# Kernel optimization log

Hardware: AMD Instinct MI355X
Metric: run time of the kernel (lower is better)

Reference implementation:

```python
import jax, jax.numpy as jnp
import numpy as np

MAX_NUM_CAPS = 10
NEG = -1e9

def _layernorm(x, g, b):
    m = x.mean(-1, keepdims=True)
    v = x.var(-1, keepdims=True)
    return (x - m) / jnp.sqrt(v + 1e-5) * g + b

def _gatv2(x, Wl, Wr, att, bias, adj):
    # x: [B,M,F]; Wl/Wr: [F,H*C]; att: [H,C]; adj: [B,M,M] bool, adj[b,i,j] = edge i->j
    B, M, F = x.shape
    H, C = att.shape
    xl = jnp.einsum('bmf,fhc->bmhc', x, Wl.reshape(F, H, C))  # source transform
    xr = jnp.einsum('bmf,fhc->bmhc', x, Wr.reshape(F, H, C))  # target transform
    # GATv2 score: att . leaky_relu(xl[i] + xr[j]) for edge (src=i, dst=j)
    z = jax.nn.leaky_relu(xl[:, :, None, :, :] + xr[:, None, :, :, :], 0.2)  # [B,i,j,H,C]
    e = jnp.einsum('bijhc,hc->bijh', z, att)
    e = jnp.where(adj[..., None], e, NEG)
    alpha = jax.nn.softmax(e, axis=1)  # softmax over incoming sources i per target j
    out = jnp.einsum('bijh,bihc->bjhc', alpha, xl)  # aggregate at targets
    return out.reshape(B, M, H * C) + bias

def setup_inputs() -> dict:
    key = jax.random.key(0)
    ks = jax.random.split(key, 16)
    B, N, T = 128, 16, 48
    Fm, H, C3 = 128, 4, 64
    s = 0.05
    inp = {
        'team_obs': jax.random.normal(ks[0], (B, N, 14), jnp.float32),
        'target_obs': jax.random.normal(ks[1], (B, T, 15), jnp.float32),
        'team_mask': jax.random.normal(ks[2], (B, 2, N), jnp.float32),
        'local_target_mask': jnp.ones((B, T + 1), jnp.float32),
        'W_emb': jax.random.normal(ks[3], (16, Fm), jnp.float32) * s,
        'b_emb': jnp.zeros((Fm,), jnp.float32),
        'Wl1': jax.random.normal(ks[4], (Fm, Fm), jnp.float32) * s,
        'Wr1': jax.random.normal(ks[5], (Fm, Fm), jnp.float32) * s,
        'att1': jax.random.normal(ks[6], (H, Fm // H), jnp.float32) * s,
        'b1': jnp.zeros((Fm,), jnp.float32),
        'Wl2': jax.random.normal(ks[7], (Fm, Fm), jnp.float32) * s,
        'Wr2': jax.random.normal(ks[8], (Fm, Fm), jnp.float32) * s,
        'att2': jax.random.normal(ks[9], (H, Fm // H), jnp.float32) * s,
        'b2': jnp.zeros((Fm,), jnp.float32),
        'Wl3': jax.random.normal(ks[10], (Fm, C3), jnp.float32) * s,
        'Wr3': jax.random.normal(ks[11], (Fm, C3), jnp.float32) * s,
        'att3': jax.random.normal(ks[12], (1, C3), jnp.float32) * s,
        'b3': jnp.zeros((C3,), jnp.float32),
        'ln1_g': jnp.ones((Fm,), jnp.float32),
        'ln1_b': jnp.zeros((Fm,), jnp.float32),
        'ln2_g': jnp.ones((Fm,), jnp.float32),
        'ln2_b': jnp.zeros((Fm,), jnp.float32),
    }
    return inp

def reference(team_obs, target_obs, team_mask, local_target_mask,
              W_emb, b_emb, Wl1, Wr1, att1, b1, Wl2, Wr2, att2, b2,
              Wl3, Wr3, att3, b3, ln1_g, ln1_b, ln2_g, ln2_b):
    B, N, _ = team_obs.shape
    team = jnp.concatenate([team_obs, jnp.zeros((B, N, 2), team_obs.dtype)], axis=2)
    tgt = target_obs[:, :, :-1]
    T = tgt.shape[1]
    tgt = jnp.concatenate([tgt[:, :, :2 + MAX_NUM_CAPS],
                           jnp.zeros((B, T, 2), tgt.dtype),
                           tgt[:, :, -2:]], axis=2)
    fin = jnp.concatenate([team, tgt], axis=1)  # [B, M, inp_dim]
    h = fin @ W_emb + b_emb  # [B, M, 128]
    imp_team = team_mask[:, 0] != -1e9          # [B, N]
    imp_tgt = local_target_mask[:, :-1] != 0.0  # [B, T]
    imp = jnp.concatenate([imp_team, imp_tgt], axis=1)  # [B, M]
    M = N + T
    eye = jnp.eye(M, dtype=bool)
    # edges among active nodes minus diagonal; PyG GATv2Conv add_self_loops=True re-adds self edges
    adj = (imp[:, :, None] & imp[:, None, :] & ~eye) | eye  # [B, M, M]
    out = jax.nn.relu(_layernorm(_gatv2(h, Wl1, Wr1, att1, b1, adj), ln1_g, ln1_b))
    out = jax.nn.relu(_layernorm(_gatv2(out, Wl2, Wr2, att2, b2, adj), ln2_g, ln2_b))
    out = _gatv2(out, Wl3, Wr3, att3, b3, adj)
    return out  # [B, M, out_dim]
```

## Files before the change

kernel.cpp:

```cpp
#include <hip/hip_runtime.h>

typedef unsigned short u16;
typedef unsigned int   u32;
typedef _Float16 h2  __attribute__((ext_vector_type(2)));
typedef __fp16   hw2 __attribute__((ext_vector_type(2)));
typedef __fp16   hw8 __attribute__((ext_vector_type(8)));
typedef float    f4  __attribute__((ext_vector_type(4)));

#define XS 136
#define PS 72
#define BS 72
#define OS 72

static __device__ __forceinline__ h2 pk(float a, float b) {
    return __builtin_bit_cast(h2, __builtin_amdgcn_cvt_pkrtz(a, b));
}
static __device__ __forceinline__ float dot2(h2 a, h2 b, float c) {
    return __builtin_amdgcn_fdot2(__builtin_bit_cast(hw2, a),
                                  __builtin_bit_cast(hw2, b), c, false);
}
static __device__ __forceinline__ h2  b2h(u32 v) { return __builtin_bit_cast(h2, v); }
static __device__ __forceinline__ u32 h2u(h2 v)  { return __builtin_bit_cast(u32, v); }
static __device__ __forceinline__ h2  abs2(h2 v) { return b2h(h2u(v) & 0x7fff7fffu); }
static __device__ __forceinline__ u16 f2h(float f) { return __builtin_bit_cast(u16, (_Float16)f); }
static __device__ __forceinline__ f4 mfma16(uint4 a, uint4 b, f4 c) {
    return __builtin_amdgcn_mfma_f32_16x16x32_f16(__builtin_bit_cast(hw8, a),
                                                  __builtin_bit_cast(hw8, b), c, 0, 0, 0);
}

__global__ void pack_weights(const float* __restrict__ Wl1, const float* __restrict__ Wr1,
                             const float* __restrict__ Wl2, const float* __restrict__ Wr2,
                             const float* __restrict__ Wl3, const float* __restrict__ Wr3,
                             u32* __restrict__ wpk)
{
    const int o = blockIdx.x * 256 + threadIdx.x;
    const float* src; u32* dst; int local; int N;
    if      (o < 8192)  { src = Wl1; dst = wpk;         local = o;         N = 128; }
    else if (o < 16384) { src = Wr1; dst = wpk + 8192;  local = o - 8192;  N = 128; }
    else if (o < 24576) { src = Wl2; dst = wpk + 16384; local = o - 16384; N = 128; }
    else if (o < 32768) { src = Wr2; dst = wpk + 24576; local = o - 24576; N = 128; }
    else if (o < 36864) { src = Wl3; dst = wpk + 32768; local = o - 32768; N = 64;  }
    else                { src = Wr3; dst = wpk + 36864; local = o - 36864; N = 64;  }
    const int i2   = local & 3;
    const int lane = (local >> 2) & 63;
    const int frag = local >> 8;
    const int kb   = frag & 3;
    const int nt   = frag >> 2;
    const int k0   = kb*32 + ((lane >> 4) << 3) + i2*2;
    const int n    = nt*16 + (lane & 15);
    dst[local] = h2u(pk(src[k0*N + n], src[(k0+1)*N + n]));
}

static __device__ __forceinline__ void compute_imp(int t, int b,
    const float* __restrict__ team_mask, const float* __restrict__ ltm, float* sImp)
{
    if (t < 64) {
        float im;
        if (t < 16) im = (team_mask[b*32 + t] != -1000000000.0f) ? 1.f : 0.f;
        else        im = (ltm[b*49 + (t-16)] != 0.0f) ? 1.f : 0.f;
        sImp[t] = im;
    }
}

static __device__ __forceinline__ void matmul128(int w, int lane,
    const u32* __restrict__ wpkL, const u32* __restrict__ wpkR,
    const u16* sX, u16* sXl, uint4* sXrP, u16* sXlB)
{
    const int  mt  = w & 3;
    const bool isR = (w >= 4);
    const u32* wp  = isR ? wpkR : wpkL;
    const int  n15 = lane & 15;
    const int  qd  = lane >> 4;
    uint4 afr[4];
#pragma unroll
    for (int kb = 0; kb < 4; kb++)
        afr[kb] = *(const uint4*)&sX[(mt*16 + n15)*XS + kb*32 + (qd << 3)];
#pragma unroll
    for (int nt = 0; nt < 8; nt++) {
        f4 acc = {0.f, 0.f, 0.f, 0.f};
#pragma unroll
        for (int kb = 0; kb < 4; kb++) {
            uint4 bf = *(const uint4*)&wp[((nt*4 + kb)*64 + lane)*4];
            acc = mfma16(afr[kb], bf, acc);
        }
        const int n  = nt*16 + n15;
        const int mb = mt*16 + (qd << 2);
        if (!isR) {
#pragma unroll
            for (int r = 0; r < 4; r++) sXl[(mb + r)*XS + n] = f2h(acc[r]);
            uint2 u;
            u.x = h2u(pk(acc[0], acc[1]));
            u.y = h2u(pk(acc[2], acc[3]));
            *(uint2*)&sXlB[n*BS + mb] = u;
        } else {
            u16* xp = (u16*)sXrP;
#pragma unroll
            for (int r = 0; r < 4; r++)
                xp[(((n >> 3)*64) + mb + r)*8 + (n & 7)] = f2h(acc[r]);
        }
    }
}

static __device__ __forceinline__ void attn_scores(int w, int lane,
    const float* __restrict__ att,
    const u16* sXl, const uint4* sXrP, u16* sP,
    float* sAl, float* sL2, const float* sImp)
{
    const int h  = w & 3;
    const int hf = w >> 2;
    const int j  = lane;

    h2 a2[16];
#pragma unroll
    for (int q = 0; q < 16; q++) a2[q] = pk(att[h*32 + 2*q], att[h*32 + 2*q + 1]);

    if (w < 4) {
        const uint4* pr = (const uint4*)&sXl[lane*XS + h*32];
        float al = 0.f;
#pragma unroll
        for (int c4 = 0; c4 < 4; c4++) {
            uint4 v = pr[c4];
            al = dot2(b2h(v.x), a2[c4*4+0], al);
            al = dot2(b2h(v.y), a2[c4*4+1], al);
            al = dot2(b2h(v.z), a2[c4*4+2], al);
            al = dot2(b2h(v.w), a2[c4*4+3], al);
        }
        sAl[h*64 + lane] = al;
    }

    h2 xr2[16];
#pragma unroll
    for (int s = 0; s < 4; s++) {
        uint4 v = sXrP[(h*4 + s)*64 + j];
        xr2[s*4+0] = b2h(v.x); xr2[s*4+1] = b2h(v.y);
        xr2[s*4+2] = b2h(v.z); xr2[s*4+3] = b2h(v.w);
    }
    float Ar = 0.f;
#pragma unroll
    for (int q = 0; q < 16; q++) Ar = dot2(a2[q], xr2[q], Ar);
    const float impj = sImp[j];
    __syncthreads();

    float l = 0.f;
    uint4* pd = (uint4*)&sP[(h*64 + j)*PS + hf*32];
    for (int c8 = 0; c8 < 4; c8++) {
        u32 pr4[4];
        float pprev = 0.f;
#pragma unroll
        for (int i2 = 0; i2 < 8; i2++) {
            const int i = hf*32 + c8*8 + i2;
            const uint4* pl = (const uint4*)&sXl[i*XS + h*32];
            uint4 v0 = pl[0], v1 = pl[1], v2 = pl[2], v3 = pl[3];
            h2 xl2[16];
            xl2[0] = b2h(v0.x); xl2[1] = b2h(v0.y); xl2[2]  = b2h(v0.z); xl2[3]  = b2h(v0.w);
            xl2[4] = b2h(v1.x); xl2[5] = b2h(v1.y); xl2[6]  = b2h(v1.z); xl2[7]  = b2h(v1.w);
            xl2[8] = b2h(v2.x); xl2[9] = b2h(v2.y); xl2[10] = b2h(v2.z); xl2[11] = b2h(v2.w);
            xl2[12]= b2h(v3.x); xl2[13]= b2h(v3.y); xl2[14] = b2h(v3.z); xl2[15] = b2h(v3.w);
            float S0 = 0.f, S1 = 0.f;
#pragma unroll
            for (int q = 0; q < 16; q += 2) {
                h2 t0 = abs2(xl2[q]   + xr2[q]);
                h2 t1 = abs2(xl2[q+1] + xr2[q+1]);
                S0 = dot2(a2[q],   t0, S0);
                S1 = dot2(a2[q+1], t1, S1);
            }
            float e  = 0.6f*(sAl[h*64 + i] + Ar) + 0.4f*(S0 + S1);
            float ad = (i == j) ? 1.f : impj * sImp[i];
            float p  = (ad != 0.f) ? __expf(e) : 0.f;
            if (i2 & 1) {
                h2 pp = pk(pprev, p);
                pr4[i2 >> 1] = h2u(pp);
                l += (float)pp[0] + (float)pp[1];
            } else {
                pprev = p;
            }
        }
        pd[c8] = make_uint4(pr4[0], pr4[1], pr4[2], pr4[3]);
    }
    sL2[h*128 + hf*64 + j] = l;
}

static __device__ __forceinline__ void attn_agg_ln(int w, int lane,
    const float* __restrict__ bias, const float* __restrict__ lg, const float* __restrict__ lb,
    const u16* sP, const u16* sXlB, float* sOutF, const float* sL2,
    float* sPart, u16* sXout)
{
    const int h   = w & 3;
    const int jh2 = w >> 2;
    const int n15 = lane & 15;
    const int kq  = lane >> 4;

    f4 acc00 = {0.f,0.f,0.f,0.f}, acc01 = acc00, acc10 = acc00, acc11 = acc00;
#pragma unroll
    for (int ks = 0; ks < 2; ks++) {
        uint4 af0 = *(const uint4*)&sP[(h*64 + (jh2*2+0)*16 + n15)*PS + ks*32 + kq*8];
        uint4 af1 = *(const uint4*)&sP[(h*64 + (jh2*2+1)*16 + n15)*PS + ks*32 + kq*8];
        uint4 bf0 = *(const uint4*)&sXlB[(h*32 +  0 + n15)*BS + ks*32 + kq*8];
        uint4 bf1 = *(const uint4*)&sXlB[(h*32 + 16 + n15)*BS + ks*32 + kq*8];
        acc00 = mfma16(af0, bf0, acc00);
        acc01 = mfma16(af0, bf1, acc01);
        acc10 = mfma16(af1, bf0, acc10);
        acc11 = mfma16(af1, bf1, acc11);
    }
    {
        const int jb0 = jh2*32 + kq*4;
#pragma unroll
        for (int r = 0; r < 4; r++) {
            sOutF[(h*32 +  0 + n15)*OS + jb0 + r]      = acc00[r];
            sOutF[(h*32 + 16 + n15)*OS + jb0 + r]      = acc01[r];
            sOutF[(h*32 +  0 + n15)*OS + jb0 + 16 + r] = acc10[r];
            sOutF[(h*32 + 16 + n15)*OS + jb0 + 16 + r] = acc11[r];
        }
    }
    __syncthreads();

    const int cg = w, j = lane, hh = w >> 1;
    const float l  = sL2[hh*128 + j] + sL2[hh*128 + 64 + j];
    const float rl = 1.f / l;
    float y[16];
    float s1 = 0.f, s2 = 0.f;
#pragma unroll
    for (int k = 0; k < 16; k++) {
        float v = fmaf(sOutF[(cg*16 + k)*OS + j], rl, bias[cg*16 + k]);
        y[k] = v; s1 += v; s2 = fmaf(v, v, s2);
    }
    sPart[cg*64 + j] = s1;
    sPart[512 + cg*64 + j] = s2;
    __syncthreads();
    float su = 0.f, sq = 0.f;
#pragma unroll
    for (int p = 0; p < 8; p++) { su += sPart[p*64 + j]; sq += sPart[512 + p*64 + j]; }
    const float mean = su * 0.0078125f;
    const float var  = sq * 0.0078125f - mean*mean;
    const float rstd = rsqrtf(var + 1e-5f);
    u32* xo = (u32*)&sXout[j*XS];
#pragma unroll
    for (int q = 0; q < 8; q++) {
        const int c0 = cg*16 + 2*q;
        float v0 = fmaxf(fmaf((y[2*q]   - mean)*rstd, lg[c0],   lb[c0]),   0.f);
        float v1 = fmaxf(fmaf((y[2*q+1] - mean)*rstd, lg[c0+1], lb[c0+1]), 0.f);
        xo[cg*8 + q] = h2u(pk(v0, v1));
    }
}

__global__ void __launch_bounds__(512, 1) gnn_fused(
    const float* __restrict__ team_obs, const float* __restrict__ target_obs,
    const float* __restrict__ team_mask, const float* __restrict__ ltm,
    const float* __restrict__ W_emb, const float* __restrict__ b_emb,
    const float* __restrict__ att1, const float* __restrict__ b1,
    const float* __restrict__ ln1_g, const float* __restrict__ ln1_b,
    const float* __restrict__ att2, const float* __restrict__ b2,
    const float* __restrict__ ln2_g, const float* __restrict__ ln2_b,
    const float* __restrict__ att3, const float* __restrict__ b3,
    const u32* __restrict__ wpk, float* __restrict__ out)
{
    __shared__ __align__(16) u16   sX  [64*XS];
    __shared__ __align__(16) u16   sXl [64*XS];
    __shared__ __align__(16) uint4 sXrP[1024];
    __shared__ __align__(16) u16   sXlB[128*BS];
    __shared__ __align__(16) u16   sP  [4*64*PS];
    __shared__ __align__(16) float sOutF[128*OS];
    __shared__ float sAl [256];
    __shared__ float sPart[1024];
    __shared__ float sL2 [768];
    __shared__ float sImp[64];

    const int t    = threadIdx.x;
    const int w    = t >> 6;
    const int lane = t & 63;
    const int b    = blockIdx.x;

    float* sFin = (float*)sP;

    compute_imp(t, b, team_mask, ltm, sImp);
    for (int ee = t; ee < 1024; ee += 512) {
        int m = ee >> 4, k = ee & 15;
        float v = 0.f;
        if (m < 16) {
            if (k < 14) v = team_obs[(b*16 + m)*14 + k];
        } else {
            const float* tg = target_obs + (size_t)(b*48 + (m-16))*15;
            if      (k < 12)  v = tg[k];
            else if (k == 14) v = tg[12];
            else if (k == 15) v = tg[13];
        }
        sFin[m*16 + k] = v;
    }
    __syncthreads();

    {
        const int f = t & 127;
        const int g = t >> 7;
        float wreg[16];
#pragma unroll
        for (int k = 0; k < 16; k++) wreg[k] = W_emb[k*128 + f];
        const float bf = b_emb[f];
#pragma unroll
        for (int mm = 0; mm < 16; mm++) {
            int m = g*16 + mm;
            const float4* pf = (const float4*)&sFin[m*16];
            float4 f0 = pf[0], f1 = pf[1], f2 = pf[2], f3 = pf[3];
            float acc = bf;
            acc = fmaf(f0.x, wreg[0],  acc); acc = fmaf(f0.y, wreg[1],  acc);
            acc = fmaf(f0.z, wreg[2],  acc); acc = fmaf(f0.w, wreg[3],  acc);
            acc = fmaf(f1.x, wreg[4],  acc); acc = fmaf(f1.y, wreg[5],  acc);
            acc = fmaf(f1.z, wreg[6],  acc); acc = fmaf(f1.w, wreg[7],  acc);
            acc = fmaf(f2.x, wreg[8],  acc); acc = fmaf(f2.y, wreg[9],  acc);
            acc = fmaf(f2.z, wreg[10], acc); acc = fmaf(f2.w, wreg[11], acc);
            acc = fmaf(f3.x, wreg[12], acc); acc = fmaf(f3.y, wreg[13], acc);
            acc = fmaf(f3.z, wreg[14], acc); acc = fmaf(f3.w, wreg[15], acc);
            sX[m*XS + f] = f2h(acc);
        }
    }
    __syncthreads();

    matmul128(w, lane, wpk, wpk + 8192, sX, sXl, sXrP, sXlB);
    __syncthreads();
    attn_scores(w, lane, att1, sXl, sXrP, sP, sAl, sL2, sImp);
    __syncthreads();
    attn_agg_ln(w, lane, b1, ln1_g, ln1_b, sP, sXlB, sOutF, sL2, sPart, sX);
    __syncthreads();

    matmul128(w, lane, wpk + 16384, wpk + 24576, sX, sXl, sXrP, sXlB);
    __syncthreads();
    attn_scores(w, lane, att2, sXl, sXrP, sP, sAl, sL2, sImp);
    __syncthreads();
    attn_agg_ln(w, lane, b2, ln2_g, ln2_b, sP, sXlB, sOutF, sL2, sPart, sX);
    __syncthreads();

    {
        const int  mt  = w & 3;
        const bool isR = (w >= 4);
        const u32* wp  = isR ? (wpk + 36864) : (wpk + 32768);
        const int  n15 = lane & 15;
        const int  qd  = lane >> 4;
        uint4 afr[4];
#pragma unroll
        for (int kb = 0; kb < 4; kb++)
            afr[kb] = *(const uint4*)&sX[(mt*16 + n15)*XS + kb*32 + (qd << 3)];
#pragma unroll
        for (int nt = 0; nt < 4; nt++) {
            f4 acc = {0.f, 0.f, 0.f, 0.f};
#pragma unroll
            for (int kb = 0; kb < 4; kb++) {
                uint4 bf = *(const uint4*)&wp[((nt*4 + kb)*64 + lane)*4];
                acc = mfma16(afr[kb], bf, acc);
            }
            const int n  = nt*16 + n15;
            const int mb = mt*16 + (qd << 2);
            if (!isR) {
#pragma unroll
                for (int r = 0; r < 4; r++) sXl[(mb + r)*XS + n] = f2h(acc[r]);
                uint2 u;
                u.x = h2u(pk(acc[0], acc[1]));
                u.y = h2u(pk(acc[2], acc[3]));
                *(uint2*)&sXlB[n*BS + mb] = u;
            } else {
                u16* xp = (u16*)sXrP;
#pragma unroll
                for (int r = 0; r < 4; r++)
                    xp[(((n >> 3)*64) + mb + r)*8 + (n & 7)] = f2h(acc[r]);
            }
        }
    }
    __syncthreads();

    {
        h2 a2l[4];
#pragma unroll
        for (int q = 0; q < 4; q++) a2l[q] = pk(att3[w*8 + 2*q], att3[w*8 + 2*q + 1]);
        uint4 v = *(const uint4*)&sXl[lane*XS + w*8];
        float al = 0.f;
        al = dot2(b2h(v.x), a2l[0], al);
        al = dot2(b2h(v.y), a2l[1], al);
        al = dot2(b2h(v.z), a2l[2], al);
        al = dot2(b2h(v.w), a2l[3], al);
        sPart[w*64 + lane] = al;
    }
    __syncthreads();
    if (t < 64) {
        sAl[t] = ((sPart[t] + sPart[64+t]) + (sPart[128+t] + sPart[192+t]))
               + ((sPart[256+t] + sPart[320+t]) + (sPart[384+t] + sPart[448+t]));
    }
    __syncthreads();

    {
        h2 a3[32], xr3[32];
#pragma unroll
        for (int q = 0; q < 32; q++) a3[q] = pk(att3[2*q], att3[2*q + 1]);
#pragma unroll
        for (int s = 0; s < 8; s++) {
            uint4 v = sXrP[s*64 + lane];
            xr3[s*4+0] = b2h(v.x); xr3[s*4+1] = b2h(v.y);
            xr3[s*4+2] = b2h(v.z); xr3[s*4+3] = b2h(v.w);
        }
        float Ar = 0.f;
#pragma unroll
        for (int q = 0; q < 32; q++) Ar = dot2(a3[q], xr3[q], Ar);
        const float impj = sImp[lane];
        float l3 = 0.f;
        u32 pr4[4];
        float pprev = 0.f;
#pragma unroll
        for (int ii = 0; ii < 8; ii++) {
            const int i = w*8 + ii;
            const uint4* pl = (const uint4*)&sXl[i*XS];
            float S0 = 0.f, S1 = 0.f;
#pragma unroll
            for (int c4 = 0; c4 < 8; c4++) {
                uint4 v = pl[c4];
                S0 = dot2(a3[c4*4+0], abs2(b2h(v.x) + xr3[c4*4+0]), S0);
                S1 = dot2(a3[c4*4+1], abs2(b2h(v.y) + xr3[c4*4+1]), S1);
                S0 = dot2(a3[c4*4+2], abs2(b2h(v.z) + xr3[c4*4+2]), S0);
                S1 = dot2(a3[c4*4+3], abs2(b2h(v.w) + xr3[c4*4+3]), S1);
            }
            float e  = 0.6f*(sAl[i] + Ar) + 0.4f*(S0 + S1);
            float ad = (i == lane) ? 1.f : impj * sImp[i];
            float p  = (ad != 0.f) ? __expf(e) : 0.f;
            if (ii & 1) {
                h2 pp = pk(pprev, p);
                pr4[ii >> 1] = h2u(pp);
                l3 += (float)pp[0] + (float)pp[1];
            } else {
                pprev = p;
            }
        }
        *(uint4*)&sP[lane*PS + w*8] = make_uint4(pr4[0], pr4[1], pr4[2], pr4[3]);
        sPart[w*64 + lane] = l3;
    }
    __syncthreads();
    if (t < 64) {
        float s = ((sPart[t] + sPart[64+t]) + (sPart[128+t] + sPart[192+t]))
                + ((sPart[256+t] + sPart[320+t]) + (sPart[384+t] + sPart[448+t]));
        sL2[t] = 1.f / s;
    }

    {
        const int jt  = w & 3;
        const int cth = w >> 2;
        const int n15 = lane & 15;
        const int kq  = lane >> 4;
        f4 acc0 = {0.f,0.f,0.f,0.f}, acc1 = acc0;
#pragma unroll
        for (int ks = 0; ks < 2; ks++) {
            uint4 af = *(const uint4*)&sP[(jt*16 + n15)*PS + ks*32 + kq*8];
            uint4 bf0 = *(const uint4*)&sXlB[((cth*2+0)*16 + n15)*BS + ks*32 + kq*8];
            uint4 bf1 = *(const uint4*)&sXlB[((cth*2+1)*16 + n15)*BS + ks*32 + kq*8];
            acc0 = mfma16(af, bf0, acc0);
            acc1 = mfma16(af, bf1, acc1);
        }
        __syncthreads();
        const int c0 = (cth*2+0)*16 + n15;
        const int c1 = (cth*2+1)*16 + n15;
        const float bc0 = b3[c0], bc1 = b3[c1];
#pragma unroll
        for (int r = 0; r < 4; r++) {
            const int jj = jt*16 + kq*4 + r;
            const float rl = sL2[jj];
            out[(size_t)b*4096 + (size_t)jj*64 + c0] = fmaf(acc0[r], rl, bc0);
            out[(size_t)b*4096 + (size_t)jj*64 + c1] = fmaf(acc1[r], rl, bc1);
        }
    }
}

extern "C" void kernel_launch(void* const* d_in, const int* in_sizes, int n_in,
                              void* d_out, int out_size, void* d_ws, size_t ws_size,
                              hipStream_t stream) {
    (void)in_sizes; (void)n_in; (void)ws_size; (void)out_size;
    const float* team_obs          = (const float*)d_in[0];
    const float* target_obs        = (const float*)d_in[1];
    const float* team_mask         = (const float*)d_in[2];
    const float* local_target_mask = (const float*)d_in[3];
    const float* W_emb             = (const float*)d_in[4];
    const float* b_emb             = (const float*)d_in[5];
    const float* Wl1               = (const float*)d_in[6];
    const float* Wr1               = (const float*)d_in[7];
    const float* att1              = (const float*)d_in[8];
    const float* b1                = (const float*)d_in[9];
    const float* Wl2               = (const float*)d_in[10];
    const float* Wr2               = (const float*)d_in[11];
    const float* att2              = (const float*)d_in[12];
    const float* b2                = (const float*)d_in[13];
    const float* Wl3               = (const float*)d_in[14];
    const float* Wr3               = (const float*)d_in[15];
    const float* att3              = (const float*)d_in[16];
    const float* b3                = (const float*)d_in[17];
    const float* ln1_g             = (const float*)d_in[18];
    const float* ln1_b             = (const float*)d_in[19];
    const float* ln2_g             = (const float*)d_in[20];
    const float* ln2_b             = (const float*)d_in[21];
    float* out = (float*)d_out;

    u32* wpk = (u32*)d_ws;

    pack_weights<<<dim3(160), dim3(256), 0, stream>>>(Wl1, Wr1, Wl2, Wr2, Wl3, Wr3, wpk);
    gnn_fused<<<dim3(128), dim3(512), 0, stream>>>(
        team_obs, target_obs, team_mask, local_target_mask, W_emb, b_emb,
        att1, b1, ln1_g, ln1_b, att2, b2, ln2_g, ln2_b, att3, b3, wpk, out);
}
```

Baseline: 143.3 us.

## Double block size to 1024 threads and split per-wave work in half

```diff
diff --git a/kernel.cpp b/kernel.cpp
--- a/kernel.cpp
+++ b/kernel.cpp
@@ -67,7 +67,8 @@
     const u16* sX, u16* sXl, uint4* sXrP, u16* sXlB)
 {
     const int  mt  = w & 3;
-    const bool isR = (w >= 4);
+    const bool isR = (w >> 2) & 1;
+    const int  nh  = w >> 3;
     const u32* wp  = isR ? wpkR : wpkL;
     const int  n15 = lane & 15;
     const int  qd  = lane >> 4;
@@ -76,7 +77,7 @@
     for (int kb = 0; kb < 4; kb++)
         afr[kb] = *(const uint4*)&sX[(mt*16 + n15)*XS + kb*32 + (qd << 3)];
 #pragma unroll
-    for (int nt = 0; nt < 8; nt++) {
+    for (int nt = nh*4; nt < nh*4 + 4; nt++) {
         f4 acc = {0.f, 0.f, 0.f, 0.f};
 #pragma unroll
         for (int kb = 0; kb < 4; kb++) {
@@ -107,7 +108,7 @@
     float* sAl, float* sL2, const float* sImp)
 {
     const int h  = w & 3;
-    const int hf = w >> 2;
+    const int qf = w >> 2;
     const int j  = lane;
 
     h2 a2[16];
@@ -142,13 +143,13 @@
     __syncthreads();
 
     float l = 0.f;
-    uint4* pd = (uint4*)&sP[(h*64 + j)*PS + hf*32];
-    for (int c8 = 0; c8 < 4; c8++) {
+    uint4* pd = (uint4*)&sP[(h*64 + j)*PS + qf*16];
+    for (int c8 = 0; c8 < 2; c8++) {
         u32 pr4[4];
         float pprev = 0.f;
 #pragma unroll
         for (int i2 = 0; i2 < 8; i2++) {
-            const int i = hf*32 + c8*8 + i2;
+            const int i = qf*16 + c8*8 + i2;
             const uint4* pl = (const uint4*)&sXl[i*XS + h*32];
             uint4 v0 = pl[0], v1 = pl[1], v2 = pl[2], v3 = pl[3];
             h2 xl2[16];
@@ -177,7 +178,7 @@
         }
         pd[c8] = make_uint4(pr4[0], pr4[1], pr4[2], pr4[3]);
     }
-    sL2[h*128 + hf*64 + j] = l;
+    sL2[h*256 + qf*64 + j] = l;
 }
 
 static __device__ __forceinline__ void attn_agg_ln(int w, int lane,
@@ -186,64 +187,60 @@
     float* sPart, u16* sXout)
 {
     const int h   = w & 3;
-    const int jh2 = w >> 2;
+    const int jq  = w >> 2;
     const int n15 = lane & 15;
     const int kq  = lane >> 4;
 
-    f4 acc00 = {0.f,0.f,0.f,0.f}, acc01 = acc00, acc10 = acc00, acc11 = acc00;
+    f4 acc0 = {0.f,0.f,0.f,0.f}, acc1 = acc0;
 #pragma unroll
     for (int ks = 0; ks < 2; ks++) {
-        uint4 af0 = *(const uint4*)&sP[(h*64 + (jh2*2+0)*16 + n15)*PS + ks*32 + kq*8];
-        uint4 af1 = *(const uint4*)&sP[(h*64 + (jh2*2+1)*16 + n15)*PS + ks*32 + kq*8];
+        uint4 af  = *(const uint4*)&sP[(h*64 + jq*16 + n15)*PS + ks*32 + kq*8];
         uint4 bf0 = *(const uint4*)&sXlB[(h*32 +  0 + n15)*BS + ks*32 + kq*8];
         uint4 bf1 = *(const uint4*)&sXlB[(h*32 + 16 + n15)*BS + ks*32 + kq*8];
-        acc00 = mfma16(af0, bf0, acc00);
-        acc01 = mfma16(af0, bf1, acc01);
-        acc10 = mfma16(af1, bf0, acc10);
-        acc11 = mfma16(af1, bf1, acc11);
-    }
-    {
-        const int jb0 = jh2*32 + kq*4;
+        acc0 = mfma16(af, bf0, acc0);
+        acc1 = mfma16(af, bf1, acc1);
+    }
+    {
+        const int jb0 = jq*16 + kq*4;
 #pragma unroll
         for (int r = 0; r < 4; r++) {
-            sOutF[(h*32 +  0 + n15)*OS + jb0 + r]      = acc00[r];
-            sOutF[(h*32 + 16 + n15)*OS + jb0 + r]      = acc01[r];
-            sOutF[(h*32 +  0 + n15)*OS + jb0 + 16 + r] = acc10[r];
-            sOutF[(h*32 + 16 + n15)*OS + jb0 + 16 + r] = acc11[r];
-        }
-    }
-    __syncthreads();
-
-    const int cg = w, j = lane, hh = w >> 1;
-    const float l  = sL2[hh*128 + j] + sL2[hh*128 + 64 + j];
+            sOutF[(h*32 +  0 + n15)*OS + jb0 + r] = acc0[r];
+            sOutF[(h*32 + 16 + n15)*OS + jb0 + r] = acc1[r];
+        }
+    }
+    __syncthreads();
+
+    const int cg = w, j = lane, hd = cg >> 2;
+    const float l  = (sL2[hd*256 + j]       + sL2[hd*256 +  64 + j])
+                   + (sL2[hd*256 + 128 + j] + sL2[hd*256 + 192 + j]);
     const float rl = 1.f / l;
-    float y[16];
+    float y[8];
     float s1 = 0.f, s2 = 0.f;
 #pragma unroll
-    for (int k = 0; k < 16; k++) {
-        float v = fmaf(sOutF[(cg*16 + k)*OS + j], rl, bias[cg*16 + k]);
+    for (int k = 0; k < 8; k++) {
+        float v = fmaf(sOutF[(cg*8 + k)*OS + j], rl, bias[cg*8 + k]);
         y[k] = v; s1 += v; s2 = fmaf(v, v, s2);
     }
-    sPart[cg*64 + j] = s1;
-    sPart[512 + cg*64 + j] = s2;
+    sPart[cg*64 + j]        = s1;
+    sPart[1024 + cg*64 + j] = s2;
     __syncthreads();
     float su = 0.f, sq = 0.f;
 #pragma unroll
-    for (int p = 0; p < 8; p++) { su += sPart[p*64 + j]; sq += sPart[512 + p*64 + j]; }
+    for (int p = 0; p < 16; p++) { su += sPart[p*64 + j]; sq += sPart[1024 + p*64 + j]; }
     const float mean = su * 0.0078125f;
     const float var  = sq * 0.0078125f - mean*mean;
     const float rstd = rsqrtf(var + 1e-5f);
     u32* xo = (u32*)&sXout[j*XS];
 #pragma unroll
-    for (int q = 0; q < 8; q++) {
-        const int c0 = cg*16 + 2*q;
+    for (int q = 0; q < 4; q++) {
+        const int c0 = cg*8 + 2*q;
         float v0 = fmaxf(fmaf((y[2*q]   - mean)*rstd, lg[c0],   lb[c0]),   0.f);
         float v1 = fmaxf(fmaf((y[2*q+1] - mean)*rstd, lg[c0+1], lb[c0+1]), 0.f);
-        xo[cg*8 + q] = h2u(pk(v0, v1));
-    }
-}
-
-__global__ void __launch_bounds__(512, 1) gnn_fused(
+        xo[cg*4 + q] = h2u(pk(v0, v1));
+    }
+}
+
+__global__ void __launch_bounds__(1024, 4) gnn_fused(
     const float* __restrict__ team_obs, const float* __restrict__ target_obs,
     const float* __restrict__ team_mask, const float* __restrict__ ltm,
     const float* __restrict__ W_emb, const float* __restrict__ b_emb,
@@ -261,8 +258,8 @@
     __shared__ __align__(16) u16   sP  [4*64*PS];
     __shared__ __align__(16) float sOutF[128*OS];
     __shared__ float sAl [256];
-    __shared__ float sPart[1024];
-    __shared__ float sL2 [768];
+    __shared__ float sPart[2048];
+    __shared__ float sL2 [1024];
     __shared__ float sImp[64];
 
     const int t    = threadIdx.x;
@@ -273,8 +270,8 @@
     float* sFin = (float*)sP;
 
     compute_imp(t, b, team_mask, ltm, sImp);
-    for (int ee = t; ee < 1024; ee += 512) {
-        int m = ee >> 4, k = ee & 15;
+    {
+        int m = t >> 4, k = t & 15;
         float v = 0.f;
         if (m < 16) {
             if (k < 14) v = team_obs[(b*16 + m)*14 + k];
@@ -296,8 +293,8 @@
         for (int k = 0; k < 16; k++) wreg[k] = W_emb[k*128 + f];
         const float bf = b_emb[f];
 #pragma unroll
-        for (int mm = 0; mm < 16; mm++) {
-            int m = g*16 + mm;
+        for (int mm = 0; mm < 8; mm++) {
+            int m = g*8 + mm;
             const float4* pf = (const float4*)&sFin[m*16];
             float4 f0 = pf[0], f1 = pf[1], f2 = pf[2], f3 = pf[3];
             float acc = bf;
@@ -330,7 +327,8 @@
 
     {
         const int  mt  = w & 3;
-        const bool isR = (w >= 4);
+        const bool isR = (w >> 2) & 1;
+        const int  nh  = w >> 3;
         const u32* wp  = isR ? (wpk + 36864) : (wpk + 32768);
         const int  n15 = lane & 15;
         const int  qd  = lane >> 4;
@@ -339,7 +337,7 @@
         for (int kb = 0; kb < 4; kb++)
             afr[kb] = *(const uint4*)&sX[(mt*16 + n15)*XS + kb*32 + (qd << 3)];
 #pragma unroll
-        for (int nt = 0; nt < 4; nt++) {
+        for (int nt = nh*2; nt < nh*2 + 2; nt++) {
             f4 acc = {0.f, 0.f, 0.f, 0.f};
 #pragma unroll
             for (int kb = 0; kb < 4; kb++) {
@@ -366,21 +364,22 @@
     __syncthreads();
 
     {
-        h2 a2l[4];
-#pragma unroll
-        for (int q = 0; q < 4; q++) a2l[q] = pk(att3[w*8 + 2*q], att3[w*8 + 2*q + 1]);
-        uint4 v = *(const uint4*)&sXl[lane*XS + w*8];
-        float al = 0.f;
-        al = dot2(b2h(v.x), a2l[0], al);
+        h2 a2l[2];
+        a2l[0] = pk(att3[w*4 + 0], att3[w*4 + 1]);
+        a2l[1] = pk(att3[w*4 + 2], att3[w*4 + 3]);
+        uint2 v = *(const uint2*)&sXl[lane*XS + w*4];
+        float al = dot2(b2h(v.x), a2l[0], 0.f);
         al = dot2(b2h(v.y), a2l[1], al);
-        al = dot2(b2h(v.z), a2l[2], al);
-        al = dot2(b2h(v.w), a2l[3], al);
         sPart[w*64 + lane] = al;
     }
     __syncthreads();
     if (t < 64) {
-        sAl[t] = ((sPart[t] + sPart[64+t]) + (sPart[128+t] + sPart[192+t]))
-               + ((sPart[256+t] + sPart[320+t]) + (sPart[384+t] + sPart[448+t]));
+        float s = 0.f;
+#pragma unroll
+        for (int p = 0; p < 16; p += 4)
+            s += ((sPart[p*64 + t] + sPart[(p+1)*64 + t]) +
+                  (sPart[(p+2)*64 + t] + sPart[(p+3)*64 + t]));
+        sAl[t] = s;
     }
     __syncthreads();
 
@@ -399,11 +398,11 @@
         for (int q = 0; q < 32; q++) Ar = dot2(a3[q], xr3[q], Ar);
         const float impj = sImp[lane];
         float l3 = 0.f;
-        u32 pr4[4];
+        u32 pr2[2];
         float pprev = 0.f;
 #pragma unroll
-        for (int ii = 0; ii < 8; ii++) {
-            const int i = w*8 + ii;
+        for (int ii = 0; ii < 4; ii++) {
+            const int i = w*4 + ii;
             const uint4* pl = (const uint4*)&sXl[i*XS];
             float S0 = 0.f, S1 = 0.f;
 #pragma unroll
@@ -419,46 +418,44 @@
             float p  = (ad != 0.f) ? __expf(e) : 0.f;
             if (ii & 1) {
                 h2 pp = pk(pprev, p);
-                pr4[ii >> 1] = h2u(pp);
+                pr2[ii >> 1] = h2u(pp);
                 l3 += (float)pp[0] + (float)pp[1];
             } else {
                 pprev = p;
             }
         }
-        *(uint4*)&sP[lane*PS + w*8] = make_uint4(pr4[0], pr4[1], pr4[2], pr4[3]);
+        *(uint2*)&sP[lane*PS + w*4] = make_uint2(pr2[0], pr2[1]);
         sPart[w*64 + lane] = l3;
     }
     __syncthreads();
     if (t < 64) {
-        float s = ((sPart[t] + sPart[64+t]) + (sPart[128+t] + sPart[192+t]))
-                + ((sPart[256+t] + sPart[320+t]) + (sPart[384+t] + sPart[448+t]));
+        float s = 0.f;
+#pragma unroll
+        for (int p = 0; p < 16; p += 4)
+            s += ((sPart[p*64 + t] + sPart[(p+1)*64 + t]) +
+                  (sPart[(p+2)*64 + t] + sPart[(p+3)*64 + t]));
         sL2[t] = 1.f / s;
     }
 
     {
         const int jt  = w & 3;
-        const int cth = w >> 2;
+        const int ct  = w >> 2;
         const int n15 = lane & 15;
         const int kq  = lane >> 4;
-        f4 acc0 = {0.f,0.f,0.f,0.f}, acc1 = acc0;
+        f4 acc = {0.f,0.f,0.f,0.f};
 #pragma unroll
         for (int ks = 0; ks < 2; ks++) {
             uint4 af = *(const uint4*)&sP[(jt*16 + n15)*PS + ks*32 + kq*8];
-            uint4 bf0 = *(const uint4*)&sXlB[((cth*2+0)*16 + n15)*BS + ks*32 + kq*8];
-            uint4 bf1 = *(const uint4*)&sXlB[((cth*2+1)*16 + n15)*BS + ks*32 + kq*8];
-            acc0 = mfma16(af, bf0, acc0);
-            acc1 = mfma16(af, bf1, acc1);
+            uint4 bf = *(const uint4*)&sXlB[(ct*16 + n15)*BS + ks*32 + kq*8];
+            acc = mfma16(af, bf, acc);
         }
         __syncthreads();
-        const int c0 = (cth*2+0)*16 + n15;
-        const int c1 = (cth*2+1)*16 + n15;
-        const float bc0 = b3[c0], bc1 = b3[c1];
+        const int c  = ct*16 + n15;
+        const float bc = b3[c];
 #pragma unroll
         for (int r = 0; r < 4; r++) {
             const int jj = jt*16 + kq*4 + r;
-            const float rl = sL2[jj];
-            out[(size_t)b*4096 + (size_t)jj*64 + c0] = fmaf(acc0[r], rl, bc0);
-            out[(size_t)b*4096 + (size_t)jj*64 + c1] = fmaf(acc1[r], rl, bc1);
+            out[(size_t)b*4096 + (size_t)jj*64 + c] = fmaf(acc[r], sL2[jj], bc);
         }
     }
 }
@@ -494,7 +491,7 @@
     u32* wpk = (u32*)d_ws;
 
     pack_weights<<<dim3(160), dim3(256), 0, stream>>>(Wl1, Wr1, Wl2, Wr2, Wl3, Wr3, wpk);
-    gnn_fused<<<dim3(128), dim3(512), 0, stream>>>(
+    gnn_fused<<<dim3(128), dim3(1024), 0, stream>>>(
         team_obs, target_obs, team_mask, local_target_mask, W_emb, b_emb,
         att1, b1, ln1_g, ln1_b, att2, b2, ln2_g, ln2_b, att3, b3, wpk, out);
 }
```

Result: faster. 133.9 us (-6.6%).
